# Kernel tuning notes

Measured on AMD Instinct MI355X. Metric: run time of the kernel, lower is better.

Reference implementation:

```python
import jax, jax.numpy as jnp
import numpy as np

B, LAT, CIN, W, K, F = 16, 512, 512, 4096, 3, 512

def setup_inputs() -> dict:
    key = jax.random.key(0)
    k1, k2, k3, k4 = jax.random.split(key, 4)
    latent = jax.random.normal(k1, (B, LAT), jnp.float32)
    content = jax.random.normal(k2, (B, CIN, W), jnp.float32)
    # glorot_uniform for affine weight
    lim = np.sqrt(6.0 / (LAT + CIN))
    affine_w = jax.random.uniform(k3, (LAT, CIN), jnp.float32, -lim, lim)
    affine_b = jnp.zeros((1, CIN), jnp.float32)
    # he_normal for conv kernel (fan_in = K*CIN)
    kernel_w = jax.random.normal(k4, (K, CIN, F), jnp.float32) * np.sqrt(2.0 / (K * CIN))
    kernel_b = jnp.zeros((1, F, 1), jnp.float32)
    return {"latent": latent, "content": content, "affine_w": affine_w,
            "affine_b": affine_b, "kernel_w": kernel_w, "kernel_b": kernel_b}

def reference(latent, content, affine_w, affine_b, kernel_w, kernel_b):
    # style affine: [B, CIN]
    affine = latent @ affine_w + affine_b
    # demod scale per (b, f): 1/sqrt(sum_{k,c} (kernel[k,c,f]*affine[b,c])^2 + 1e-8)
    demod = jax.lax.rsqrt(jnp.einsum('kcf,bc->bf', kernel_w * kernel_w,
                                     affine * affine) + 1e-8)
    # modulate input instead of per-sample weights (mathematically identical,
    # avoids batch-as-groups grouped conv): x[b,c,w] = content * affine[b,c]
    x = content * affine[:, :, None]
    # shared-kernel conv1d, NCW / SAME; filter layout [K, CIN, F] == HIO
    y = jax.lax.conv_general_dilated(
        x, kernel_w, window_strides=(1,), padding='SAME',
        dimension_numbers=('NCH', 'HIO', 'NCH'))
    y = y * demod[:, :, None] + kernel_b  # [B, F, W]
    return jnp.where(y >= 0, y, 0.2 * y)  # leaky_relu(0.2)
```

## Files before the change

### kernel.cpp

```cpp
#include <hip/hip_runtime.h>
#include <hip/hip_bf16.h>

#define Bn   16
#define LATn 512
#define Cn   512
#define Wn   4096
#define Fn   512

using bf16x8 = __attribute__((ext_vector_type(8))) short;
using f32x4  = __attribute__((ext_vector_type(4))) float;

__device__ __forceinline__ unsigned short f2bf(float x) {
    union { float f; unsigned int u; } v; v.f = x;
    unsigned int r = v.u + 0x7fffu + ((v.u >> 16) & 1u);
    return (unsigned short)(r >> 16);
}

__device__ __forceinline__ void gload_lds16(const void* g, void* l) {
    __builtin_amdgcn_global_load_lds(
        (const __attribute__((address_space(1))) unsigned int*)g,
        (__attribute__((address_space(3))) unsigned int*)l, 16, 0, 0);
}

__global__ void k_affine(const float* __restrict__ latent,
                         const float* __restrict__ aw,
                         const float* __restrict__ ab,
                         float* __restrict__ affine) {
    __shared__ float red[4][64];
    const int t  = threadIdx.x;
    const int cl = t & 63, lq = t >> 6;
    const int c  = blockIdx.x * 64 + cl;
    const int b  = blockIdx.y;
    float s = 0.f;
    #pragma unroll 4
    for (int l = lq * 128; l < lq * 128 + 128; ++l)
        s = fmaf(latent[b * LATn + l], aw[(size_t)l * Cn + c], s);
    red[lq][cl] = s;
    __syncthreads();
    if (t < 64)
        affine[b * Cn + blockIdx.x * 64 + t] =
            red[0][t] + red[1][t] + red[2][t] + red[3][t] + ab[blockIdx.x * 64 + t];
}

__global__ __launch_bounds__(256)
void k_mid(const float* __restrict__ kw,
           const float* __restrict__ affine,
           const float* __restrict__ content,
           float* __restrict__ demod,
           unsigned short* __restrict__ kt,
           unsigned short* __restrict__ xh) {
    __shared__ __align__(16) char shraw[9216];
    const int t   = threadIdx.x;
    const int bid = blockIdx.x;

    if (bid < 128) {
        float (*red)[64] = (float(*)[64])shraw;
        const int fl = t & 63, cq = t >> 6;
        const int f  = (bid & 7) * 64 + fl;
        const int b  = bid >> 3;
        float s = 0.f;
        for (int c = cq * 128; c < cq * 128 + 128; ++c) {
            const float a  = affine[b * Cn + c];
            const float k0 = kw[((size_t)(0 * Cn + c)) * Fn + f];
            const float k1 = kw[((size_t)(1 * Cn + c)) * Fn + f];
            const float k2 = kw[((size_t)(2 * Cn + c)) * Fn + f];
            s = fmaf(k0 * k0 + k1 * k1 + k2 * k2, a * a, s);
        }
        red[cq][fl] = s;
        __syncthreads();
        if (t < 64)
            demod[b * Fn + (bid & 7) * 64 + t] =
                rsqrtf(red[0][t] + red[1][t] + red[2][t] + red[3][t] + 1e-8f);
    } else if (bid < 512) {
        float (*lds)[65] = (float(*)[65])shraw;
        const int e  = bid - 128;
        const int k  = e / 128;
        const int e2 = e % 128;
        const int c0 = (e2 & 15) * 32;
        const int f0 = (e2 >> 4) * 64;
        #pragma unroll
        for (int i = 0; i < 8; ++i) {
            int q = t + 256 * i; int c = q >> 6; int f = q & 63;
            lds[c][f] = kw[((size_t)(k * Cn + c0 + c)) * Fn + f0 + f];
        }
        __syncthreads();
        #pragma unroll
        for (int i = 0; i < 8; ++i) {
            int q = t + 256 * i; int f = q >> 5; int c = q & 31;
            kt[((size_t)(k * Fn + f0 + f)) * Cn + c0 + c] = f2bf(lds[c][f]);
        }
    } else {
        const int e  = bid - 512;
        const int b  = e >> 4;
        const int wb = e & 15;
        #pragma unroll
        for (int i = 0; i < 4; ++i) {
            const int idx = t + 256 * i;
            const int h   = idx >> 9;
            const int c   = idx & 511;
            const int wg  = wb * 256 + (h ? 256 : -1);
            float v = 0.f;
            if ((unsigned)wg < (unsigned)Wn)
                v = content[((size_t)(b * Cn + c)) * Wn + wg] * affine[b * Cn + c];
            xh[(((size_t)(b * 16 + wb)) * 2 + h) * 512 + c] = f2bf(v);
        }
    }
}

#define BM 256
#define BN 256
#define BK 32
#define KBYTES   (3 * BM * BK * 2)
#define BUFB     (KBYTES + BN * BK * 2)
#define HALO_OFF (2 * BUFB)
#define ALDS_OFF (HALO_OFF + 2048)
#define SMEMB    (ALDS_OFF + 2048)

extern __shared__ __align__(16) char smem[];

#define LOAD_C(c0s) { \
    _Pragma("unroll") for (int j_ = 0; j_ < 16; ++j_) \
        cbuf[j_] = content[((size_t)(b * Cn + (c0s) + cg * 16 + j_)) * Wn + w0 + wq]; }

#define WRITE_X(dst, c0s) { \
    const float* al_ = (const float*)(smem + ALDS_OFF) + (c0s) + cg * 16; \
    unsigned short h_[16]; \
    _Pragma("unroll") for (int j_ = 0; j_ < 16; ++j_) \
        h_[j_] = f2bf(cbuf[j_] * al_[j_]); \
    _Pragma("unroll") for (int i_ = 0; i_ < 2; ++i_) { \
        const int jj_ = cg * 2 + i_; \
        *(uint4*)((dst) + KBYTES + (size_t)wq * 64 + ((jj_ ^ ((wq >> 1) & 3)) * 16)) \
            = *(const uint4*)(h_ + i_ * 8); } }

#define ISSUE_PLANE(dst, c0s, P) { \
    _Pragma("unroll") for (int i_ = 0; i_ < 2; ++i_) { \
        const int Q_ = i_ * 512 + t; \
        const int r_ = (Q_ >> 2) & 255; \
        const int j_ = (Q_ & 3) ^ ((r_ >> 1) & 3); \
        gload_lds16(&kt[((size_t)((P) * Fn + f0 + r_)) * Cn + (c0s) + j_ * 8], \
                    (dst) + (size_t)((P) * 1024 + Q_) * 16); } }

#define PHASE(K, VM, ...) { \
    asm volatile("s_waitcnt vmcnt(" #VM ")" ::: "memory"); \
    asm volatile("s_barrier" ::: "memory"); \
    bf16x8 af[8]; bf16x8 bv[4]; \
    _Pragma("unroll") for (int m_ = 0; m_ < 8; ++m_) { \
        const int r_ = wm * 128 + m_ * 16 + l15; \
        af[m_] = *(const bf16x8*)(ka + ((K) * 256 + r_) * 32 + (lhi ^ ((r_ >> 1) & 3)) * 8); } \
    _Pragma("unroll") for (int n_ = 0; n_ < 4; ++n_) { \
        const int rl_ = wn * 64 + n_ * 16 + l15 + (K) - 1; \
        const unsigned short* bp_ = xa + rl_ * 32 + (lhi ^ ((rl_ >> 1) & 3)) * 8; \
        if ((K) == 0 && n_ == 0 && rl_ < 0)   bp_ = halo + c0 + lhi * 8; \
        if ((K) == 2 && n_ == 3 && rl_ > 255) bp_ = halo + 512 + c0 + lhi * 8; \
        bv[n_] = *(const bf16x8*)bp_; } \
    __VA_ARGS__; \
    asm volatile("s_waitcnt lgkmcnt(0)" ::: "memory"); \
    __builtin_amdgcn_sched_barrier(0); \
    __builtin_amdgcn_s_setprio(1); \
    _Pragma("unroll") for (int n_ = 0; n_ < 4; ++n_) \
        _Pragma("unroll") for (int m_ = 0; m_ < 8; ++m_) \
            acc[m_][n_] = __builtin_amdgcn_mfma_f32_16x16x32_bf16(af[m_], bv[n_], acc[m_][n_], 0, 0, 0); \
    __builtin_amdgcn_s_setprio(0); }

__global__ __launch_bounds__(512, 1)
void k_conv(const unsigned short* __restrict__ kt,
            const float* __restrict__ content,
            const float* __restrict__ affine,
            const unsigned short* __restrict__ xh,
            const float* __restrict__ demod,
            const float* __restrict__ kb,
            float* __restrict__ y) {
    const int t  = threadIdx.x;
    const int w0 = blockIdx.x * BN;
    const int f0 = blockIdx.y * BM;
    const int b  = blockIdx.z;

    const int wave = t >> 6;
    const int lane = t & 63;
    const int wm   = wave >> 2;
    const int wn   = wave & 3;
    const int l15  = lane & 15;
    const int lhi  = lane >> 4;
    const int cg   = t >> 8;
    const int wq   = t & 255;

    unsigned short* halo = (unsigned short*)(smem + HALO_OFF);

    f32x4 acc[8][4];
    #pragma unroll
    for (int m = 0; m < 8; ++m)
        #pragma unroll
        for (int n = 0; n < 4; ++n)
            #pragma unroll
            for (int r = 0; r < 4; ++r)
                acc[m][n][r] = 0.f;

    float cbuf[16];

    {
        float av = affine[b * Cn + t];
        ((float*)(smem + ALDS_OFF))[t] = av;
    }
    asm volatile("s_waitcnt lgkmcnt(0)" ::: "memory");
    asm volatile("s_barrier" ::: "memory");
    if (t < 128) {
        const int h = t >> 6, c8 = (t & 63) * 8;
        gload_lds16(&xh[(((size_t)(b * 16 + blockIdx.x)) * 2 + h) * 512 + c8],
                    halo + (size_t)h * 512 + c8);
    }
    LOAD_C(0);
    ISSUE_PLANE(smem, 0, 0);
    ISSUE_PLANE(smem, 0, 1);
    ISSUE_PLANE(smem, 0, 2);
    asm volatile("s_waitcnt vmcnt(6)" ::: "memory");
    WRITE_X(smem, 0);
    asm volatile("s_waitcnt lgkmcnt(0)" ::: "memory");

    int cur = 0;
    for (int cc = 0; cc < Cn / BK - 1; ++cc) {
        const unsigned short* ka = (const unsigned short*)(smem + cur * BUFB);
        const unsigned short* xa = ka + 3 * BM * BK;
        char* nbuf = smem + (cur ^ 1) * BUFB;
        const int c0 = cc * BK;
        const int c1 = c0 + BK;
        PHASE(0, 4,  LOAD_C(c1);)
        PHASE(1, 18, ISSUE_PLANE(nbuf, c1, 0); ISSUE_PLANE(nbuf, c1, 1);)
        PHASE(2, 4,  ISSUE_PLANE(nbuf, c1, 2); WRITE_X(nbuf, c1);)
        cur ^= 1;
    }
    {
        const unsigned short* ka = (const unsigned short*)(smem + cur * BUFB);
        const unsigned short* xa = ka + 3 * BM * BK;
        const int c0 = Cn - BK;
        PHASE(0, 4, )
        PHASE(1, 2, )
        PHASE(2, 0, )
    }

    #pragma unroll
    for (int m = 0; m < 8; ++m) {
        const int fb = f0 + wm * 128 + m * 16 + lhi * 4;
        const float4 dmv = *(const float4*)&demod[b * Fn + fb];
        const float4 kbv = *(const float4*)&kb[fb];
        const float dmf[4] = {dmv.x, dmv.y, dmv.z, dmv.w};
        const float kbf[4] = {kbv.x, kbv.y, kbv.z, kbv.w};
        #pragma unroll
        for (int n = 0; n < 4; ++n) {
            const int w = w0 + wn * 64 + n * 16 + l15;
            #pragma unroll
            for (int r = 0; r < 4; ++r) {
                float v = fmaf(acc[m][n][r], dmf[r], kbf[r]);
                v = (v >= 0.f) ? v : 0.2f * v;
                y[((size_t)(b * Fn + fb + r)) * Wn + w] = v;
            }
        }
    }
}

extern "C" void kernel_launch(void* const* d_in, const int* in_sizes, int n_in,
                              void* d_out, int out_size, void* d_ws, size_t ws_size,
                              hipStream_t stream) {
    const float* latent  = (const float*)d_in[0];
    const float* content = (const float*)d_in[1];
    const float* aw      = (const float*)d_in[2];
    const float* ab      = (const float*)d_in[3];
    const float* kw      = (const float*)d_in[4];
    const float* kb      = (const float*)d_in[5];
    float* y = (float*)d_out;

    char* ws = (char*)d_ws;
    float*          affine = (float*)(ws);
    float*          demod  = (float*)(ws + 32768);
    unsigned short* kt     = (unsigned short*)(ws + 131072);
    unsigned short* xh     = (unsigned short*)(ws + 2u * 1024u * 1024u);
    if (ws_size < 3u * 1024u * 1024u) return;

    hipFuncSetAttribute((const void*)k_conv,
                        hipFuncAttributeMaxDynamicSharedMemorySize, SMEMB);

    k_affine<<<dim3(Cn / 64, Bn),          256, 0, stream>>>(latent, aw, ab, affine);
    k_mid   <<<dim3(128 + 384 + 256),      256, 0, stream>>>(kw, affine, content, demod, kt, xh);
    k_conv  <<<dim3(Wn / BN, Fn / BM, Bn), 512, SMEMB, stream>>>(kt, content, affine, xh, demod, kb, y);
}
```

Before: 146.0 us.

## Double-buffer content register loads one K-tile ahead in conv pipeline

```diff
diff --git a/kernel.cpp b/kernel.cpp
--- a/kernel.cpp
+++ b/kernel.cpp
@@ -118,15 +118,15 @@
 
 extern __shared__ __align__(16) char smem[];
 
-#define LOAD_C(c0s) { \
+#define LOAD_C(c0s, CB) { \
     _Pragma("unroll") for (int j_ = 0; j_ < 16; ++j_) \
-        cbuf[j_] = content[((size_t)(b * Cn + (c0s) + cg * 16 + j_)) * Wn + w0 + wq]; }
-
-#define WRITE_X(dst, c0s) { \
+        CB[j_] = content[((size_t)(b * Cn + (c0s) + cg * 16 + j_)) * Wn + w0 + wq]; }
+
+#define WRITE_X(dst, c0s, CB) { \
     const float* al_ = (const float*)(smem + ALDS_OFF) + (c0s) + cg * 16; \
     unsigned short h_[16]; \
     _Pragma("unroll") for (int j_ = 0; j_ < 16; ++j_) \
-        h_[j_] = f2bf(cbuf[j_] * al_[j_]); \
+        h_[j_] = f2bf(CB[j_] * al_[j_]); \
     _Pragma("unroll") for (int i_ = 0; i_ < 2; ++i_) { \
         const int jj_ = cg * 2 + i_; \
         *(uint4*)((dst) + KBYTES + (size_t)wq * 64 + ((jj_ ^ ((wq >> 1) & 3)) * 16)) \
@@ -162,6 +162,18 @@
             acc[m_][n_] = __builtin_amdgcn_mfma_f32_16x16x32_bf16(af[m_], bv[n_], acc[m_][n_], 0, 0, 0); \
     __builtin_amdgcn_s_setprio(0); }
 
+#define TILE_BODY(c0v, CBCONS, CBLOAD, DOLOAD) { \
+    const unsigned short* ka = (const unsigned short*)(smem + cur * BUFB); \
+    const unsigned short* xa = ka + 3 * BM * BK; \
+    char* nbuf = smem + (cur ^ 1) * BUFB; \
+    const int c0 = (c0v); \
+    const int c1 = c0 + BK; \
+    PHASE(0, 20, ) \
+    PHASE(1, 18, ISSUE_PLANE(nbuf, c1, 0); ISSUE_PLANE(nbuf, c1, 1);) \
+    PHASE(2, 4,  ISSUE_PLANE(nbuf, c1, 2); WRITE_X(nbuf, c1, CBCONS); \
+                 if (DOLOAD) { LOAD_C(c1 + BK, CBLOAD); }) \
+    cur ^= 1; }
+
 __global__ __launch_bounds__(512, 1)
 void k_conv(const unsigned short* __restrict__ kt,
             const float* __restrict__ content,
@@ -195,12 +207,9 @@
             for (int r = 0; r < 4; ++r)
                 acc[m][n][r] = 0.f;
 
-    float cbuf[16];
-
-    {
-        float av = affine[b * Cn + t];
-        ((float*)(smem + ALDS_OFF))[t] = av;
-    }
+    float cbufA[16], cbufB[16];
+
+    ((float*)(smem + ALDS_OFF))[t] = affine[b * Cn + t];
     asm volatile("s_waitcnt lgkmcnt(0)" ::: "memory");
     asm volatile("s_barrier" ::: "memory");
     if (t < 128) {
@@ -208,26 +217,21 @@
         gload_lds16(&xh[(((size_t)(b * 16 + blockIdx.x)) * 2 + h) * 512 + c8],
                     halo + (size_t)h * 512 + c8);
     }
-    LOAD_C(0);
+    LOAD_C(0, cbufA);
     ISSUE_PLANE(smem, 0, 0);
     ISSUE_PLANE(smem, 0, 1);
     ISSUE_PLANE(smem, 0, 2);
-    asm volatile("s_waitcnt vmcnt(6)" ::: "memory");
-    WRITE_X(smem, 0);
+    asm volatile("s_waitcnt vmcnt(0)" ::: "memory");
+    WRITE_X(smem, 0, cbufA);
+    LOAD_C(BK, cbufB);
     asm volatile("s_waitcnt lgkmcnt(0)" ::: "memory");
 
     int cur = 0;
-    for (int cc = 0; cc < Cn / BK - 1; ++cc) {
-        const unsigned short* ka = (const unsigned short*)(smem + cur * BUFB);
-        const unsigned short* xa = ka + 3 * BM * BK;
-        char* nbuf = smem + (cur ^ 1) * BUFB;
-        const int c0 = cc * BK;
-        const int c1 = c0 + BK;
-        PHASE(0, 4,  LOAD_C(c1);)
-        PHASE(1, 18, ISSUE_PLANE(nbuf, c1, 0); ISSUE_PLANE(nbuf, c1, 1);)
-        PHASE(2, 4,  ISSUE_PLANE(nbuf, c1, 2); WRITE_X(nbuf, c1);)
-        cur ^= 1;
-    }
+    for (int pp = 0; pp < 7; ++pp) {
+        TILE_BODY(pp * 64,      cbufB, cbufA, true)
+        TILE_BODY(pp * 64 + 32, cbufA, cbufB, true)
+    }
+    TILE_BODY(14 * BK, cbufB, cbufA, false)
     {
         const unsigned short* ka = (const unsigned short*)(smem + cur * BUFB);
         const unsigned short* xa = ka + 3 * BM * BK;
```

Result: slower. 392.5 us (+168.8%).

## Split conv kernel into producer waves for loads and consumer waves for MFMA

Applied to the files above, without the earlier changes.

```diff
diff --git a/kernel.cpp b/kernel.cpp
--- a/kernel.cpp
+++ b/kernel.cpp
@@ -113,35 +113,33 @@
 #define KBYTES   (3 * BM * BK * 2)
 #define BUFB     (KBYTES + BN * BK * 2)
 #define HALO_OFF (2 * BUFB)
-#define ALDS_OFF (HALO_OFF + 2048)
-#define SMEMB    (ALDS_OFF + 2048)
+#define SMEMB    (HALO_OFF + 2048)
 
 extern __shared__ __align__(16) char smem[];
 
-#define LOAD_C(c0s) { \
-    _Pragma("unroll") for (int j_ = 0; j_ < 16; ++j_) \
-        cbuf[j_] = content[((size_t)(b * Cn + (c0s) + cg * 16 + j_)) * Wn + w0 + wq]; }
-
-#define WRITE_X(dst, c0s) { \
-    const float* al_ = (const float*)(smem + ALDS_OFF) + (c0s) + cg * 16; \
-    unsigned short h_[16]; \
-    _Pragma("unroll") for (int j_ = 0; j_ < 16; ++j_) \
-        h_[j_] = f2bf(cbuf[j_] * al_[j_]); \
-    _Pragma("unroll") for (int i_ = 0; i_ < 2; ++i_) { \
-        const int jj_ = cg * 2 + i_; \
-        *(uint4*)((dst) + KBYTES + (size_t)wq * 64 + ((jj_ ^ ((wq >> 1) & 3)) * 16)) \
-            = *(const uint4*)(h_ + i_ * 8); } }
-
-#define ISSUE_PLANE(dst, c0s, P) { \
-    _Pragma("unroll") for (int i_ = 0; i_ < 2; ++i_) { \
-        const int Q_ = i_ * 512 + t; \
+#define STAGE_A(dst, c0s) { \
+    _Pragma("unroll") for (int i_ = 0; i_ < 12; ++i_) { \
+        const int Q_ = i_ * 256 + pid; \
+        const int P_ = Q_ >> 10; \
         const int r_ = (Q_ >> 2) & 255; \
         const int j_ = (Q_ & 3) ^ ((r_ >> 1) & 3); \
-        gload_lds16(&kt[((size_t)((P) * Fn + f0 + r_)) * Cn + (c0s) + j_ * 8], \
-                    (dst) + (size_t)((P) * 1024 + Q_) * 16); } }
-
-#define PHASE(K, VM, ...) { \
-    asm volatile("s_waitcnt vmcnt(" #VM ")" ::: "memory"); \
+        gload_lds16(&kt[((size_t)(P_ * Fn + f0 + r_)) * Cn + (c0s) + j_ * 8], \
+                    (dst) + (size_t)Q_ * 16); } }
+
+#define LOAD_CP(c0s) { \
+    _Pragma("unroll") for (int j_ = 0; j_ < 32; ++j_) \
+        cbuf[j_] = content[((size_t)(b * Cn + (c0s) + j_)) * Wn + w0 + pid]; }
+
+#define WRITE_XP(dst, c0s) { \
+    unsigned short h_[32]; \
+    _Pragma("unroll") for (int j_ = 0; j_ < 32; ++j_) \
+        h_[j_] = f2bf(cbuf[j_] * affine[b * Cn + (c0s) + j_]); \
+    _Pragma("unroll") for (int i_ = 0; i_ < 4; ++i_) { \
+        const int jj_ = i_ ^ ((pid >> 1) & 3); \
+        *(uint4*)((dst) + KBYTES + (size_t)pid * 64 + jj_ * 16) \
+            = *(const uint4*)(h_ + i_ * 8); } }
+
+#define CPHASE(K) { \
     asm volatile("s_barrier" ::: "memory"); \
     bf16x8 af[8]; bf16x8 bv[4]; \
     _Pragma("unroll") for (int m_ = 0; m_ < 8; ++m_) { \
@@ -153,7 +151,6 @@
         if ((K) == 0 && n_ == 0 && rl_ < 0)   bp_ = halo + c0 + lhi * 8; \
         if ((K) == 2 && n_ == 3 && rl_ > 255) bp_ = halo + 512 + c0 + lhi * 8; \
         bv[n_] = *(const bf16x8*)bp_; } \
-    __VA_ARGS__; \
     asm volatile("s_waitcnt lgkmcnt(0)" ::: "memory"); \
     __builtin_amdgcn_sched_barrier(0); \
     __builtin_amdgcn_s_setprio(1); \
@@ -162,7 +159,7 @@
             acc[m_][n_] = __builtin_amdgcn_mfma_f32_16x16x32_bf16(af[m_], bv[n_], acc[m_][n_], 0, 0, 0); \
     __builtin_amdgcn_s_setprio(0); }
 
-__global__ __launch_bounds__(512, 1)
+__global__ __launch_bounds__(768, 3)
 void k_conv(const unsigned short* __restrict__ kt,
             const float* __restrict__ content,
             const float* __restrict__ affine,
@@ -174,17 +171,46 @@
     const int w0 = blockIdx.x * BN;
     const int f0 = blockIdx.y * BM;
     const int b  = blockIdx.z;
-
     const int wave = t >> 6;
+
+    unsigned short* halo = (unsigned short*)(smem + HALO_OFF);
+
+    if (wave >= 8) {
+        const int pid = t - 512;
+        float cbuf[32];
+
+        if (pid < 128) {
+            const int h = pid >> 6, c8 = (pid & 63) * 8;
+            gload_lds16(&xh[(((size_t)(b * 16 + blockIdx.x)) * 2 + h) * 512 + c8],
+                        halo + (size_t)h * 512 + c8);
+        }
+        STAGE_A(smem, 0);
+        LOAD_CP(0);
+        asm volatile("s_waitcnt vmcnt(0)" ::: "memory");
+        WRITE_XP(smem, 0);
+        asm volatile("s_waitcnt lgkmcnt(0)" ::: "memory");
+
+        for (int tt = 0; tt < 16; ++tt) {
+            char* nbuf = smem + ((tt + 1) & 1) * BUFB;
+            const int c1 = (tt + 1) * BK;
+            asm volatile("s_barrier" ::: "memory");
+            if (tt < 15) { STAGE_A(nbuf, c1); LOAD_CP(c1); }
+            asm volatile("s_barrier" ::: "memory");
+            if (tt < 15) {
+                asm volatile("s_waitcnt vmcnt(0)" ::: "memory");
+                WRITE_XP(nbuf, c1);
+                asm volatile("s_waitcnt lgkmcnt(0)" ::: "memory");
+            }
+            asm volatile("s_barrier" ::: "memory");
+        }
+        return;
+    }
+
     const int lane = t & 63;
     const int wm   = wave >> 2;
     const int wn   = wave & 3;
     const int l15  = lane & 15;
     const int lhi  = lane >> 4;
-    const int cg   = t >> 8;
-    const int wq   = t & 255;
-
-    unsigned short* halo = (unsigned short*)(smem + HALO_OFF);
 
     f32x4 acc[8][4];
     #pragma unroll
@@ -195,46 +221,13 @@
             for (int r = 0; r < 4; ++r)
                 acc[m][n][r] = 0.f;
 
-    float cbuf[16];
-
-    {
-        float av = affine[b * Cn + t];
-        ((float*)(smem + ALDS_OFF))[t] = av;
-    }
-    asm volatile("s_waitcnt lgkmcnt(0)" ::: "memory");
-    asm volatile("s_barrier" ::: "memory");
-    if (t < 128) {
-        const int h = t >> 6, c8 = (t & 63) * 8;
-        gload_lds16(&xh[(((size_t)(b * 16 + blockIdx.x)) * 2 + h) * 512 + c8],
-                    halo + (size_t)h * 512 + c8);
-    }
-    LOAD_C(0);
-    ISSUE_PLANE(smem, 0, 0);
-    ISSUE_PLANE(smem, 0, 1);
-    ISSUE_PLANE(smem, 0, 2);
-    asm volatile("s_waitcnt vmcnt(6)" ::: "memory");
-    WRITE_X(smem, 0);
-    asm volatile("s_waitcnt lgkmcnt(0)" ::: "memory");
-
-    int cur = 0;
-    for (int cc = 0; cc < Cn / BK - 1; ++cc) {
-        const unsigned short* ka = (const unsigned short*)(smem + cur * BUFB);
+    for (int cc = 0; cc < Cn / BK; ++cc) {
+        const unsigned short* ka = (const unsigned short*)(smem + (cc & 1) * BUFB);
         const unsigned short* xa = ka + 3 * BM * BK;
-        char* nbuf = smem + (cur ^ 1) * BUFB;
         const int c0 = cc * BK;
-        const int c1 = c0 + BK;
-        PHASE(0, 4,  LOAD_C(c1);)
-        PHASE(1, 18, ISSUE_PLANE(nbuf, c1, 0); ISSUE_PLANE(nbuf, c1, 1);)
-        PHASE(2, 4,  ISSUE_PLANE(nbuf, c1, 2); WRITE_X(nbuf, c1);)
-        cur ^= 1;
-    }
-    {
-        const unsigned short* ka = (const unsigned short*)(smem + cur * BUFB);
-        const unsigned short* xa = ka + 3 * BM * BK;
-        const int c0 = Cn - BK;
-        PHASE(0, 4, )
-        PHASE(1, 2, )
-        PHASE(2, 0, )
+        CPHASE(0)
+        CPHASE(1)
+        CPHASE(2)
     }
 
     #pragma unroll
@@ -280,5 +273,5 @@
 
     k_affine<<<dim3(Cn / 64, Bn),          256, 0, stream>>>(latent, aw, ab, affine);
     k_mid   <<<dim3(128 + 384 + 256),      256, 0, stream>>>(kw, affine, content, demod, kt, xh);
-    k_conv  <<<dim3(Wn / BN, Fn / BM, Bn), 512, SMEMB, stream>>>(kt, content, affine, xh, demod, kb, y);
-}
+    k_conv  <<<dim3(Wn / BN, Fn / BM, Bn), 768, SMEMB, stream>>>(kt, content, affine, xh, demod, kb, y);
+}
```

Result: slower. 389.2 us (+166.5%).
